# Kernel tuning notes

Hardware: AMD Instinct MI355X
Metric: run time of the kernel (lower is better)

## Reference

```python
import jax, jax.numpy as jnp
import numpy as np

B, C, H, W = 4, 512, 56, 56
G, K = 16, 3
P = K * K
GC = C // G
DWK = 3
PAD = 1
OFFSET_SCALE = 1.0


def setup_inputs():
    key = jax.random.key(0)
    ks = jax.random.split(key, 10)

    def w(i, shape, sc=0.02):
        return jax.random.normal(ks[i], shape, jnp.float32) * sc

    return {
        "x": jax.random.normal(ks[0], (B, C, H, W), jnp.float32),
        "w_in": w(1, (C, C)), "b_in": jnp.zeros((C,), jnp.float32),
        "w_dw": w(2, (DWK, DWK, 1, C)), "b_dw": jnp.zeros((C,), jnp.float32),
        "ln_g": jnp.ones((C,), jnp.float32), "ln_b": jnp.zeros((C,), jnp.float32),
        "w_off": w(3, (C, G * P * 2)), "b_off": jnp.zeros((G * P * 2,), jnp.float32),
        "w_mask": w(4, (C, G * P)), "b_mask": jnp.zeros((G * P,), jnp.float32),
        "w_out": w(5, (C, C)), "b_out": jnp.zeros((C,), jnp.float32),
        "bn_g": jnp.ones((C,), jnp.float32), "bn_b": jnp.zeros((C,), jnp.float32),
        "bn_m": w(6, (C,), 0.1), "bn_v": jnp.abs(w(7, (C,), 0.1)) + 1.0,
    }


def _dcnv3_core(xp, offset, mask):
    """xp: [B,H,W,C]; offset: [B,H,W,G*P*2]; mask (softmaxed over P): [B,H,W,G,P]."""
    xpad = jnp.pad(xp, ((0, 0), (PAD, PAD), (PAD, PAD), (0, 0)))
    Hin, Win = H + 2 * PAD, W + 2 * PAD
    # normalized reference points (output-location centers in padded input coords)
    ref_x = (jnp.arange(W, dtype=jnp.float32) + 0.5 + (K - 1) // 2) / Win
    ref_y = (jnp.arange(H, dtype=jnp.float32) + 0.5 + (K - 1) // 2) / Hin
    # dilation grid, kx-major / ky-minor flattening (matches InternImage core)
    k = jnp.arange(K, dtype=jnp.float32) - (K - 1) // 2
    gx = jnp.repeat(k, K) / Win  # [P]
    gy = jnp.tile(k, K) / Hin    # [P]
    off = offset.reshape(B, H, W, G, P, 2)
    lx = ref_x[None, None, :, None, None] + gx * OFFSET_SCALE + off[..., 0] * OFFSET_SCALE / Win
    ly = ref_y[None, :, None, None, None] + gy * OFFSET_SCALE + off[..., 1] * OFFSET_SCALE / Hin
    # grid_sample semantics, align_corners=False, zero padding
    px = lx * Win - 0.5
    py = ly * Hin - 0.5
    x0f = jnp.floor(px)
    y0f = jnp.floor(py)
    tx = px - x0f
    ty = py - y0f
    x0 = x0f.astype(jnp.int32)
    y0 = y0f.astype(jnp.int32)
    flat = xpad.reshape(B, Hin * Win * G, GC)
    gidx = jnp.arange(G)[None, None, :, None]

    def corner(fb, yi, xi):
        valid = (yi >= 0) & (yi < Hin) & (xi >= 0) & (xi < Win)
        idx = (jnp.clip(yi, 0, Hin - 1) * Win + jnp.clip(xi, 0, Win - 1)) * G + gidx
        return jnp.take(fb, idx, axis=0) * valid[..., None]  # [H,W,G,P,GC]

    def sample_one(fb, y0b, x0b, tyb, txb):
        w00 = ((1 - tyb) * (1 - txb))[..., None]
        w01 = ((1 - tyb) * txb)[..., None]
        w10 = (tyb * (1 - txb))[..., None]
        w11 = (tyb * txb)[..., None]
        return (corner(fb, y0b, x0b) * w00 + corner(fb, y0b, x0b + 1) * w01
                + corner(fb, y0b + 1, x0b) * w10 + corner(fb, y0b + 1, x0b + 1) * w11)

    samp = jax.vmap(sample_one)(flat, y0, x0, ty, tx)  # [B,H,W,G,P,GC]
    return jnp.einsum('bhwgpc,bhwgp->bhwgc', samp, mask).reshape(B, H, W, C)


def reference(x, w_in, b_in, w_dw, b_dw, ln_g, ln_b, w_off, b_off, w_mask, b_mask, w_out, b_out, bn_g, bn_b, bn_m, bn_v):
    xh = jnp.transpose(x, (0, 2, 3, 1))  # NCHW -> NHWC
    xp = xh @ w_in + b_in                # input_proj
    # offset/mask branch: depthwise conv + LayerNorm(channels) + GELU
    x1 = jax.lax.conv_general_dilated(xh, w_dw, (1, 1), 'SAME', feature_group_count=C,
                                      dimension_numbers=('NHWC', 'HWIO', 'NHWC')) + b_dw
    mu = x1.mean(-1, keepdims=True)
    var = x1.var(-1, keepdims=True)
    x1 = (x1 - mu) / jnp.sqrt(var + 1e-6) * ln_g + ln_b
    x1 = jax.nn.gelu(x1, approximate=False)
    offset = x1 @ w_off + b_off
    mask = jax.nn.softmax((x1 @ w_mask + b_mask).reshape(B, H, W, G, P), axis=-1)
    y = _dcnv3_core(xp, offset, mask)
    y = y @ w_out + b_out                # output_proj
    y = jnp.transpose(y, (0, 3, 1, 2))   # NHWC -> NCHW
    # BatchNorm2d (inference: running stats) + SiLU
    y = (y - bn_m[:, None, None]) / jnp.sqrt(bn_v[:, None, None] + 1e-5) * bn_g[:, None, None] + bn_b[:, None, None]
    return jax.nn.silu(y)
```

## Files before the change

### kernel.cpp

```cpp
#include <hip/hip_runtime.h>
#include <cmath>

constexpr int B_ = 4, C_ = 512, H_ = 56, W_ = 56;
constexpr int HW_ = H_ * W_;
constexpr int NPIX = B_ * HW_;
constexpr int G_ = 16, P_ = 9;
constexpr int NMSK = G_ * P_;

typedef __attribute__((ext_vector_type(8))) short short8;
typedef __attribute__((ext_vector_type(4))) float f32x4;

__device__ __forceinline__ float b2f(ushort u) {
    union { unsigned int i; float f; } v; v.i = (unsigned int)u << 16; return v.f;
}
__device__ __forceinline__ ushort f2b(float f) {
    unsigned int x = __float_as_uint(f);
    unsigned int r = (x + 0x7fffu + ((x >> 16) & 1u)) >> 16;
    return (ushort)r;
}
__device__ __forceinline__ void gload16(const ushort* g, ushort* l) {
    __builtin_amdgcn_global_load_lds(
        (const __attribute__((address_space(1))) unsigned int*)g,
        (__attribute__((address_space(3))) unsigned int*)l, 16, 0, 0);
}

__global__ __launch_bounds__(256) void prep_weights_kernel(
    const float* __restrict__ w_in, const float* __restrict__ w_off,
    const float* __restrict__ w_mask, const float* __restrict__ w_out,
    const float* __restrict__ b_off, const float* __restrict__ b_mask,
    ushort* __restrict__ wtA, ushort* __restrict__ wtOM, ushort* __restrict__ wtO,
    float* __restrict__ bOM)
{
    __shared__ float tile[32][33];
    int z = blockIdx.z;
    int k0 = blockIdx.x * 32;
    int n0 = blockIdx.y * 32;
    int tx = threadIdx.x, ty = threadIdx.y;
    for (int i = ty; i < 32; i += 8) {
        int k = k0 + i, n = n0 + tx;
        float v;
        if (z == 0) v = w_in[k * 512 + n];
        else if (z == 1) v = w_out[k * 512 + n];
        else v = (n < 288) ? w_off[k * 288 + n]
                           : (n < 432 ? w_mask[k * 144 + (n - 288)] : 0.f);
        tile[i][tx] = v;
    }
    __syncthreads();
    ushort* dst = (z == 0) ? wtA : (z == 1 ? wtO : wtOM);
    for (int i = ty; i < 32; i += 8)
        dst[(size_t)(n0 + i) * 512 + k0 + tx] = f2b(tile[tx][i]);
    if (z == 2 && blockIdx.x == 0 && blockIdx.y == 0) {
        int t = ty * 32 + tx;
        for (int tt = t; tt < 512; tt += 256)
            bOM[tt] = (tt < 288) ? b_off[tt] : (tt < 432 ? b_mask[tt - 288] : 0.f);
    }
}

__global__ __launch_bounds__(256) void transpose_in_kernel(
    const float* __restrict__ in, ushort* __restrict__ out)
{
    __shared__ float tile[32][33];
    int b = blockIdx.z;
    int hw0 = blockIdx.x * 32;
    int c0 = blockIdx.y * 32;
    int tx = threadIdx.x, ty = threadIdx.y;
    const float* ib = in + (size_t)b * C_ * HW_;
    #pragma unroll
    for (int i = ty; i < 32; i += 8)
        tile[i][tx] = ib[(size_t)(c0 + i) * HW_ + hw0 + tx];
    __syncthreads();
    ushort* ob = out + (size_t)b * HW_ * C_;
    #pragma unroll
    for (int i = ty; i < 32; i += 8)
        ob[(size_t)(hw0 + i) * C_ + c0 + tx] = f2b(tile[tx][i]);
}

template <int MODE>
__global__ __launch_bounds__(256) void mfma_gemm_kernel(
    const ushort* __restrict__ A, const ushort* __restrict__ Bt,
    const float* __restrict__ bias, void* __restrict__ Cout,
    const float* __restrict__ bng, const float* __restrict__ bnb,
    const float* __restrict__ bnm, const float* __restrict__ bnv)
{
    __shared__ ushort As[128 * 64];
    __shared__ ushort Bs[128 * 64];
    int tid = threadIdx.x;
    int lane = tid & 63, wid = tid >> 6;
    int bid = blockIdx.x;
    int wgid = (bid & 7) * 49 + (bid >> 3);
    int row0 = (wgid >> 2) * 128, col0 = (wgid & 3) * 128;
    int wm = wid >> 1, wn = wid & 1;

    f32x4 acc[4][4] = {};

    int lr = lane >> 3;
    int sc = (lane & 7) ^ lr;

    for (int k0 = 0; k0 < 512; k0 += 64) {
        if (k0) __syncthreads();
        #pragma unroll
        for (int i = 0; i < 4; i++) {
            int rb = (wid * 4 + i) * 8;
            gload16(A + (size_t)(row0 + rb + lr) * 512 + k0 + sc * 8, &As[rb * 64]);
            gload16(Bt + (size_t)(col0 + rb + lr) * 512 + k0 + sc * 8, &Bs[rb * 64]);
        }
        __syncthreads();
        #pragma unroll
        for (int ks = 0; ks < 2; ks++) {
            short8 af[4], bf[4];
            #pragma unroll
            for (int mi = 0; mi < 4; mi++) {
                int r = wm * 64 + mi * 16 + (lane & 15);
                int c = ((lane >> 4) + ks * 4) ^ (r & 7);
                af[mi] = *(const short8*)((const char*)As + r * 128 + c * 16);
            }
            #pragma unroll
            for (int ni = 0; ni < 4; ni++) {
                int r = wn * 64 + ni * 16 + (lane & 15);
                int c = ((lane >> 4) + ks * 4) ^ (r & 7);
                bf[ni] = *(const short8*)((const char*)Bs + r * 128 + c * 16);
            }
            #pragma unroll
            for (int mi = 0; mi < 4; mi++)
                #pragma unroll
                for (int ni = 0; ni < 4; ni++)
                    acc[mi][ni] = __builtin_amdgcn_mfma_f32_16x16x32_bf16(
                        af[mi], bf[ni], acc[mi][ni], 0, 0, 0);
        }
    }

    if constexpr (MODE == 2) {
        __shared__ float ebuf[4][32][65];
        int n_lane = row0 + wm * 64 + lane;
        int bb = n_lane / HW_;
        int hww = n_lane - bb * HW_;
        size_t obase = (size_t)bb * C_ * HW_ + hww;
        #pragma unroll
        for (int half = 0; half < 2; half++) {
            #pragma unroll
            for (int ni2 = 0; ni2 < 2; ni2++) {
                int ni = half * 2 + ni2;
                int col = col0 + wn * 64 + ni * 16 + (lane & 15);
                float bv = bias[col];
                float inv = rsqrtf(bnv[col] + 1e-5f);
                float bsc = bng[col] * inv;
                float bsh = bnb[col] - bnm[col] * bsc;
                int cl = ni2 * 16 + (lane & 15);
                int rl = (lane >> 4) * 4;
                #pragma unroll
                for (int mi = 0; mi < 4; mi++)
                    #pragma unroll
                    for (int r = 0; r < 4; r++) {
                        float val = acc[mi][ni][r] + bv;
                        float t2 = val * bsc + bsh;
                        float s = t2 / (1.f + expf(-t2));
                        ebuf[wid][cl][mi * 16 + rl + r] = s;
                    }
            }
            __syncthreads();
            #pragma unroll
            for (int c = 0; c < 32; c++) {
                int chan = col0 + wn * 64 + half * 32 + c;
                ((float*)Cout)[obase + (size_t)chan * HW_] = ebuf[wid][c][lane];
            }
            __syncthreads();
        }
    } else {
        #pragma unroll
        for (int ni = 0; ni < 4; ni++) {
            int col = col0 + wn * 64 + ni * 16 + (lane & 15);
            float bv = bias[col];
            #pragma unroll
            for (int mi = 0; mi < 4; mi++) {
                int rowb = row0 + wm * 64 + mi * 16 + (lane >> 4) * 4;
                #pragma unroll
                for (int r = 0; r < 4; r++) {
                    float val = acc[mi][ni][r] + bv;
                    if constexpr (MODE == 0)
                        ((float*)Cout)[(size_t)(rowb + r) * 512 + col] = val;
                    else
                        ((ushort*)Cout)[(size_t)(rowb + r) * 512 + col] = f2b(val);
                }
            }
        }
    }
}

__global__ __launch_bounds__(256) void dwln_kernel(
    const ushort* __restrict__ xh, const float* __restrict__ wdw,
    const float* __restrict__ bdw, const float* __restrict__ lng,
    const float* __restrict__ lnb, ushort* __restrict__ x1)
{
    int tid = threadIdx.x;
    int wid = tid >> 6, lane = tid & 63;
    int n = blockIdx.x * 4 + wid;
    int b = n / HW_, hw = n % HW_;
    int h = hw / W_, w = hw % W_;
    int c0 = lane * 8;
    const ushort* base = xh + (size_t)b * HW_ * C_ + c0;

    uint4 nb[9];
    #pragma unroll
    for (int ky = 0; ky < 3; ky++)
        #pragma unroll
        for (int kx = 0; kx < 3; kx++) {
            int hh = h + ky - 1, ww = w + kx - 1;
            bool ok = (hh >= 0) & (hh < H_) & (ww >= 0) & (ww < W_);
            nb[ky * 3 + kx] = ok ? *(const uint4*)(base + ((size_t)hh * W_ + ww) * C_)
                                 : make_uint4(0u, 0u, 0u, 0u);
        }

    float acc[8];
    {
        float4 b0 = *(const float4*)&bdw[c0];
        float4 b1 = *(const float4*)&bdw[c0 + 4];
        acc[0] = b0.x; acc[1] = b0.y; acc[2] = b0.z; acc[3] = b0.w;
        acc[4] = b1.x; acc[5] = b1.y; acc[6] = b1.z; acc[7] = b1.w;
    }
    #pragma unroll
    for (int p = 0; p < 9; p++) {
        float4 w0 = *(const float4*)&wdw[p * C_ + c0];
        float4 w1 = *(const float4*)&wdw[p * C_ + c0 + 4];
        float wv[8] = {w0.x, w0.y, w0.z, w0.w, w1.x, w1.y, w1.z, w1.w};
        unsigned int u[4] = {nb[p].x, nb[p].y, nb[p].z, nb[p].w};
        #pragma unroll
        for (int q = 0; q < 4; q++) {
            float lo = __uint_as_float(u[q] << 16);
            float hi = __uint_as_float(u[q] & 0xffff0000u);
            acc[2 * q]     += wv[2 * q]     * lo;
            acc[2 * q + 1] += wv[2 * q + 1] * hi;
        }
    }

    float s1 = 0.f, s2 = 0.f;
    #pragma unroll
    for (int q = 0; q < 8; q++) { s1 += acc[q]; s2 += acc[q] * acc[q]; }
    #pragma unroll
    for (int o = 32; o > 0; o >>= 1) {
        s1 += __shfl_xor(s1, o);
        s2 += __shfl_xor(s2, o);
    }
    float mean = s1 * (1.f / 512.f);
    float var = s2 * (1.f / 512.f) - mean * mean;
    float inv = rsqrtf(var + 1e-6f);

    float4 g0 = *(const float4*)&lng[c0];
    float4 g1 = *(const float4*)&lng[c0 + 4];
    float4 e0 = *(const float4*)&lnb[c0];
    float4 e1 = *(const float4*)&lnb[c0 + 4];
    float gv[8] = {g0.x, g0.y, g0.z, g0.w, g1.x, g1.y, g1.z, g1.w};
    float ev[8] = {e0.x, e0.y, e0.z, e0.w, e1.x, e1.y, e1.z, e1.w};
    unsigned int outw[4];
    #pragma unroll
    for (int q = 0; q < 4; q++) {
        float t0 = (acc[2 * q]     - mean) * inv * gv[2 * q]     + ev[2 * q];
        float t1 = (acc[2 * q + 1] - mean) * inv * gv[2 * q + 1] + ev[2 * q + 1];
        float ge0 = 0.5f * t0 * (1.f + erff(t0 * 0.70710678118654752f));
        float ge1 = 0.5f * t1 * (1.f + erff(t1 * 0.70710678118654752f));
        outw[q] = (unsigned int)f2b(ge0) | ((unsigned int)f2b(ge1) << 16);
    }
    *(uint4*)&x1[(size_t)n * C_ + c0] = make_uint4(outw[0], outw[1], outw[2], outw[3]);
}

__global__ __launch_bounds__(256) void dcn_sample_kernel(
    const ushort* __restrict__ xp, const ushort* __restrict__ om,
    ushort* __restrict__ y1)
{
    __shared__ float slog[NMSK];
    __shared__ float sw4[NMSK][4];
    __shared__ int   sa4[NMSK][4];
    int bid = blockIdx.x;
    int n = (bid & 7) * (NPIX / 8) + (bid >> 3);
    int b = n / HW_, hw = n % HW_;
    int h = hw / W_, w = hw % W_;
    int tid = threadIdx.x;
    const ushort* omp = om + (size_t)n * 512;

    if (tid < NMSK) slog[tid] = b2f(omp[288 + tid]);
    __syncthreads();
    if (tid < G_) {
        float mx = -1e30f;
        #pragma unroll
        for (int p = 0; p < P_; p++) mx = fmaxf(mx, slog[tid * P_ + p]);
        float e[P_], s = 0.f;
        #pragma unroll
        for (int p = 0; p < P_; p++) { e[p] = expf(slog[tid * P_ + p] - mx); s += e[p]; }
        float invs = 1.f / s;
        #pragma unroll
        for (int p = 0; p < P_; p++) slog[tid * P_ + p] = e[p] * invs;
    }
    __syncthreads();
    if (tid < NMSK) {
        int g = tid / 9, p = tid - g * 9;
        float ox = b2f(omp[g * 18 + p * 2 + 0]);
        float oy = b2f(omp[g * 18 + p * 2 + 1]);
        float px = (float)(w + (p / 3)) + ox;
        float py = (float)(h + (p % 3)) + oy;
        float x0f = floorf(px), y0f = floorf(py);
        float tx = px - x0f, ty = py - y0f;
        int x0 = (int)x0f, y0 = (int)y0f;
        float m = slog[tid];
        float ww[4] = { (1.f - ty) * (1.f - tx) * m, (1.f - ty) * tx * m,
                        ty * (1.f - tx) * m,         ty * tx * m };
        #pragma unroll
        for (int i = 0; i < 4; i++) {
            int yy = y0 + (i >> 1), xx = x0 + (i & 1);
            bool valid = (yy >= 1 && yy <= H_ && xx >= 1 && xx <= W_);
            sa4[tid][i] = valid ? ((yy - 1) * W_ + (xx - 1)) * C_ : 0;
            sw4[tid][i] = valid ? ww[i] : 0.f;
        }
    }
    __syncthreads();

    const ushort* xpb = xp + (size_t)b * HW_ * C_;
    int c0 = tid * 2;
    int g = tid >> 4;

    int addr[P_][4];
    #pragma unroll
    for (int p = 0; p < P_; p++)
        #pragma unroll
        for (int i = 0; i < 4; i++)
            addr[p][i] = sa4[g * 9 + p][i] + c0;

    unsigned int v[P_][4];
    #pragma unroll
    for (int p = 0; p < P_; p++)
        #pragma unroll
        for (int i = 0; i < 4; i++)
            v[p][i] = *(const unsigned int*)(xpb + addr[p][i]);

    float ax = 0.f, ay = 0.f;
    #pragma unroll
    for (int p = 0; p < P_; p++)
        #pragma unroll
        for (int i = 0; i < 4; i++) {
            float wgt = sw4[g * 9 + p][i];
            float lo = __uint_as_float(v[p][i] << 16);
            float hi = __uint_as_float(v[p][i] & 0xffff0000u);
            ax += wgt * lo;
            ay += wgt * hi;
        }

    ushort2 o; o.x = f2b(ax); o.y = f2b(ay);
    *(ushort2*)&y1[(size_t)n * 512 + c0] = o;
}

extern "C" void kernel_launch(void* const* d_in, const int* in_sizes, int n_in,
                              void* d_out, int out_size, void* d_ws, size_t ws_size,
                              hipStream_t stream)
{
    const float* x      = (const float*)d_in[0];
    const float* w_in   = (const float*)d_in[1];
    const float* b_in   = (const float*)d_in[2];
    const float* w_dw   = (const float*)d_in[3];
    const float* b_dw   = (const float*)d_in[4];
    const float* ln_g   = (const float*)d_in[5];
    const float* ln_b   = (const float*)d_in[6];
    const float* w_off  = (const float*)d_in[7];
    const float* b_off  = (const float*)d_in[8];
    const float* w_mask = (const float*)d_in[9];
    const float* b_mask = (const float*)d_in[10];
    const float* w_out  = (const float*)d_in[11];
    const float* b_out  = (const float*)d_in[12];
    const float* bn_g   = (const float*)d_in[13];
    const float* bn_b   = (const float*)d_in[14];
    const float* bn_m   = (const float*)d_in[15];
    const float* bn_v   = (const float*)d_in[16];
    float* out = (float*)d_out;

    const size_t NC = (size_t)NPIX * C_;
    char* wsp = (char*)d_ws;
    ushort* xh  = (ushort*)wsp;  wsp += NC * 2;
    ushort* x1  = (ushort*)wsp;  wsp += NC * 2;
    ushort* xpb = (ushort*)wsp;  wsp += NC * 2;
    ushort* om  = (ushort*)wsp;  wsp += NC * 2;
    ushort* wtA = (ushort*)wsp;  wsp += 512 * 512 * 2;
    ushort* wtOM= (ushort*)wsp;  wsp += 512 * 512 * 2;
    ushort* wtO = (ushort*)wsp;  wsp += 512 * 512 * 2;
    float*  bOM = (float*)wsp;   wsp += 512 * 4;

    dim3 tb(32, 8);
    prep_weights_kernel<<<dim3(16, 16, 3), tb, 0, stream>>>(
        w_in, w_off, w_mask, w_out, b_off, b_mask, wtA, wtOM, wtO, bOM);

    transpose_in_kernel<<<dim3(HW_ / 32, C_ / 32, B_), tb, 0, stream>>>(x, xh);

    mfma_gemm_kernel<1><<<392, 256, 0, stream>>>(
        xh, wtA, b_in, xpb, nullptr, nullptr, nullptr, nullptr);

    dwln_kernel<<<NPIX / 4, 256, 0, stream>>>(xh, w_dw, b_dw, ln_g, ln_b, x1);

    mfma_gemm_kernel<1><<<392, 256, 0, stream>>>(
        x1, wtOM, bOM, om, nullptr, nullptr, nullptr, nullptr);

    dcn_sample_kernel<<<NPIX, 256, 0, stream>>>(xpb, om, x1 );

    mfma_gemm_kernel<2><<<392, 256, 0, stream>>>(
        x1, wtO, b_out, out, bn_g, bn_b, bn_m, bn_v);
}
```

Baseline: 117.6 us.

## Double-buffer GEMM LDS, swizzle dwln blocks, process two pixels per DCN block

The GEMM kernel now double-buffers its LDS tiles, issuing the next K-slice's global-to-LDS loads before computing the current one, and reuses the same shared memory through a union for the epilogue buffer. The dwln kernel gets an XCD-style block index swizzle. The deformable sampling kernel handles two pixels per block with 4 channels per thread and 8-byte gathers, halving the grid and the per-pixel setup cost. Double buffering doubles LDS use per block, which may lower occupancy.

```diff
diff --git a/kernel.cpp b/kernel.cpp
--- a/kernel.cpp
+++ b/kernel.cpp
@@ -82,8 +82,11 @@
     const float* __restrict__ bng, const float* __restrict__ bnb,
     const float* __restrict__ bnm, const float* __restrict__ bnv)
 {
-    __shared__ ushort As[128 * 64];
-    __shared__ ushort Bs[128 * 64];
+    union SMem {
+        ushort ab[2][2][128 * 64];
+        float  eb[4][32][68];
+    };
+    __shared__ SMem sm;
     int tid = threadIdx.x;
     int lane = tid & 63, wid = tid >> 6;
     int bid = blockIdx.x;
@@ -96,15 +99,24 @@
     int lr = lane >> 3;
     int sc = (lane & 7) ^ lr;
 
-    for (int k0 = 0; k0 < 512; k0 += 64) {
-        if (k0) __syncthreads();
+    auto stage = [&](int buf, int k0) {
         #pragma unroll
         for (int i = 0; i < 4; i++) {
             int rb = (wid * 4 + i) * 8;
-            gload16(A + (size_t)(row0 + rb + lr) * 512 + k0 + sc * 8, &As[rb * 64]);
-            gload16(Bt + (size_t)(col0 + rb + lr) * 512 + k0 + sc * 8, &Bs[rb * 64]);
-        }
-        __syncthreads();
+            gload16(A + (size_t)(row0 + rb + lr) * 512 + k0 + sc * 8,
+                    &sm.ab[buf][0][rb * 64]);
+            gload16(Bt + (size_t)(col0 + rb + lr) * 512 + k0 + sc * 8,
+                    &sm.ab[buf][1][rb * 64]);
+        }
+    };
+
+    stage(0, 0);
+    __syncthreads();
+
+    #pragma unroll
+    for (int t = 0; t < 8; t++) {
+        int cur = t & 1;
+        if (t < 7) stage(cur ^ 1, (t + 1) * 64);
         #pragma unroll
         for (int ks = 0; ks < 2; ks++) {
             short8 af[4], bf[4];
@@ -112,13 +124,13 @@
             for (int mi = 0; mi < 4; mi++) {
                 int r = wm * 64 + mi * 16 + (lane & 15);
                 int c = ((lane >> 4) + ks * 4) ^ (r & 7);
-                af[mi] = *(const short8*)((const char*)As + r * 128 + c * 16);
+                af[mi] = *(const short8*)((const char*)sm.ab[cur][0] + r * 128 + c * 16);
             }
             #pragma unroll
             for (int ni = 0; ni < 4; ni++) {
                 int r = wn * 64 + ni * 16 + (lane & 15);
                 int c = ((lane >> 4) + ks * 4) ^ (r & 7);
-                bf[ni] = *(const short8*)((const char*)Bs + r * 128 + c * 16);
+                bf[ni] = *(const short8*)((const char*)sm.ab[cur][1] + r * 128 + c * 16);
             }
             #pragma unroll
             for (int mi = 0; mi < 4; mi++)
@@ -127,10 +139,10 @@
                     acc[mi][ni] = __builtin_amdgcn_mfma_f32_16x16x32_bf16(
                         af[mi], bf[ni], acc[mi][ni], 0, 0, 0);
         }
+        __syncthreads();
     }
 
     if constexpr (MODE == 2) {
-        __shared__ float ebuf[4][32][65];
         int n_lane = row0 + wm * 64 + lane;
         int bb = n_lane / HW_;
         int hww = n_lane - bb * HW_;
@@ -154,14 +166,14 @@
                         float val = acc[mi][ni][r] + bv;
                         float t2 = val * bsc + bsh;
                         float s = t2 / (1.f + expf(-t2));
-                        ebuf[wid][cl][mi * 16 + rl + r] = s;
+                        sm.eb[wid][cl][mi * 16 + rl + r] = s;
                     }
             }
             __syncthreads();
             #pragma unroll
             for (int c = 0; c < 32; c++) {
                 int chan = col0 + wn * 64 + half * 32 + c;
-                ((float*)Cout)[obase + (size_t)chan * HW_] = ebuf[wid][c][lane];
+                ((float*)Cout)[obase + (size_t)chan * HW_] = sm.eb[wid][c][lane];
             }
             __syncthreads();
         }
@@ -193,7 +205,9 @@
 {
     int tid = threadIdx.x;
     int wid = tid >> 6, lane = tid & 63;
-    int n = blockIdx.x * 4 + wid;
+    int bid = blockIdx.x;
+    int j = (bid & 7) * (NPIX / 32) + (bid >> 3);
+    int n = j * 4 + wid;
     int b = n / HW_, hw = n % HW_;
     int h = hw / W_, w = hw % W_;
     int c0 = lane * 8;
@@ -266,32 +280,39 @@
     const ushort* __restrict__ xp, const ushort* __restrict__ om,
     ushort* __restrict__ y1)
 {
-    __shared__ float slog[NMSK];
-    __shared__ float sw4[NMSK][4];
-    __shared__ int   sa4[NMSK][4];
+    __shared__ float slog[2][NMSK];
+    __shared__ float sw4[2][NMSK][4];
+    __shared__ int   sa4[2][NMSK][4];
     int bid = blockIdx.x;
-    int n = (bid & 7) * (NPIX / 8) + (bid >> 3);
-    int b = n / HW_, hw = n % HW_;
-    int h = hw / W_, w = hw % W_;
+    int j = (bid & 7) * (NPIX / 16) + (bid >> 3);
+    int n0 = j * 2;
     int tid = threadIdx.x;
-    const ushort* omp = om + (size_t)n * 512;
-
-    if (tid < NMSK) slog[tid] = b2f(omp[288 + tid]);
-    __syncthreads();
-    if (tid < G_) {
+
+    for (int i = tid; i < 2 * NMSK; i += 256) {
+        int pl = (i >= NMSK), idx = i - pl * NMSK;
+        slog[pl][idx] = b2f(om[(size_t)(n0 + pl) * 512 + 288 + idx]);
+    }
+    __syncthreads();
+    if (tid < 2 * G_) {
+        int pl = tid >> 4, g = tid & 15;
         float mx = -1e30f;
         #pragma unroll
-        for (int p = 0; p < P_; p++) mx = fmaxf(mx, slog[tid * P_ + p]);
+        for (int p = 0; p < P_; p++) mx = fmaxf(mx, slog[pl][g * P_ + p]);
         float e[P_], s = 0.f;
         #pragma unroll
-        for (int p = 0; p < P_; p++) { e[p] = expf(slog[tid * P_ + p] - mx); s += e[p]; }
+        for (int p = 0; p < P_; p++) { e[p] = expf(slog[pl][g * P_ + p] - mx); s += e[p]; }
         float invs = 1.f / s;
         #pragma unroll
-        for (int p = 0; p < P_; p++) slog[tid * P_ + p] = e[p] * invs;
-    }
-    __syncthreads();
-    if (tid < NMSK) {
-        int g = tid / 9, p = tid - g * 9;
+        for (int p = 0; p < P_; p++) slog[pl][g * P_ + p] = e[p] * invs;
+    }
+    __syncthreads();
+    for (int i = tid; i < 2 * NMSK; i += 256) {
+        int pl = (i >= NMSK), t = i - pl * NMSK;
+        int g = t / 9, p = t - g * 9;
+        int n = n0 + pl;
+        int hw = n % HW_;
+        int h = hw / W_, w = hw - h * W_;
+        const ushort* omp = om + (size_t)n * 512;
         float ox = b2f(omp[g * 18 + p * 2 + 0]);
         float oy = b2f(omp[g * 18 + p * 2 + 1]);
         float px = (float)(w + (p / 3)) + ox;
@@ -299,51 +320,55 @@
         float x0f = floorf(px), y0f = floorf(py);
         float tx = px - x0f, ty = py - y0f;
         int x0 = (int)x0f, y0 = (int)y0f;
-        float m = slog[tid];
+        float m = slog[pl][t];
         float ww[4] = { (1.f - ty) * (1.f - tx) * m, (1.f - ty) * tx * m,
                         ty * (1.f - tx) * m,         ty * tx * m };
         #pragma unroll
-        for (int i = 0; i < 4; i++) {
-            int yy = y0 + (i >> 1), xx = x0 + (i & 1);
+        for (int q = 0; q < 4; q++) {
+            int yy = y0 + (q >> 1), xx = x0 + (q & 1);
             bool valid = (yy >= 1 && yy <= H_ && xx >= 1 && xx <= W_);
-            sa4[tid][i] = valid ? ((yy - 1) * W_ + (xx - 1)) * C_ : 0;
-            sw4[tid][i] = valid ? ww[i] : 0.f;
-        }
-    }
-    __syncthreads();
-
-    const ushort* xpb = xp + (size_t)b * HW_ * C_;
-    int c0 = tid * 2;
-    int g = tid >> 4;
+            sa4[pl][t][q] = valid ? ((yy - 1) * W_ + (xx - 1)) * C_ : 0;
+            sw4[pl][t][q] = valid ? ww[q] : 0.f;
+        }
+    }
+    __syncthreads();
+
+    int pl = tid >> 7;
+    int lt = tid & 127;
+    int c0 = lt * 4;
+    int g = lt >> 3;
+    int n = n0 + pl;
+    const ushort* xpb = xp + (size_t)(n / HW_) * HW_ * C_;
 
     int addr[P_][4];
     #pragma unroll
     for (int p = 0; p < P_; p++)
         #pragma unroll
-        for (int i = 0; i < 4; i++)
-            addr[p][i] = sa4[g * 9 + p][i] + c0;
-
-    unsigned int v[P_][4];
+        for (int q = 0; q < 4; q++)
+            addr[p][q] = sa4[pl][g * 9 + p][q] + c0;
+
+    uint2 v[P_][4];
     #pragma unroll
     for (int p = 0; p < P_; p++)
         #pragma unroll
-        for (int i = 0; i < 4; i++)
-            v[p][i] = *(const unsigned int*)(xpb + addr[p][i]);
-
-    float ax = 0.f, ay = 0.f;
+        for (int q = 0; q < 4; q++)
+            v[p][q] = *(const uint2*)(xpb + addr[p][q]);
+
+    float a0 = 0.f, a1 = 0.f, a2 = 0.f, a3 = 0.f;
     #pragma unroll
     for (int p = 0; p < P_; p++)
         #pragma unroll
-        for (int i = 0; i < 4; i++) {
-            float wgt = sw4[g * 9 + p][i];
-            float lo = __uint_as_float(v[p][i] << 16);
-            float hi = __uint_as_float(v[p][i] & 0xffff0000u);
-            ax += wgt * lo;
-            ay += wgt * hi;
-        }
-
-    ushort2 o; o.x = f2b(ax); o.y = f2b(ay);
-    *(ushort2*)&y1[(size_t)n * 512 + c0] = o;
+        for (int q = 0; q < 4; q++) {
+            float wgt = sw4[pl][g * 9 + p][q];
+            a0 += wgt * __uint_as_float(v[p][q].x << 16);
+            a1 += wgt * __uint_as_float(v[p][q].x & 0xffff0000u);
+            a2 += wgt * __uint_as_float(v[p][q].y << 16);
+            a3 += wgt * __uint_as_float(v[p][q].y & 0xffff0000u);
+        }
+
+    ushort4 o;
+    o.x = f2b(a0); o.y = f2b(a1); o.z = f2b(a2); o.w = f2b(a3);
+    *(ushort4*)&y1[(size_t)n * 512 + c0] = o;
 }
 
 extern "C" void kernel_launch(void* const* d_in, const int* in_sizes, int n_in,
@@ -394,7 +419,7 @@
     mfma_gemm_kernel<1><<<392, 256, 0, stream>>>(
         x1, wtOM, bOM, om, nullptr, nullptr, nullptr, nullptr);
 
-    dcn_sample_kernel<<<NPIX, 256, 0, stream>>>(xpb, om, x1 );
+    dcn_sample_kernel<<<NPIX / 2, 256, 0, stream>>>(xpb, om, x1 );
 
     mfma_gemm_kernel<2><<<392, 256, 0, stream>>>(
         x1, wtO, b_out, out, bn_g, bn_b, bn_m, bn_v);
```

Result: slower. 143.1 us (+21.6%).
